# Kernel tuning notes

Measured on AMD Instinct MI355X. Metric: run time of the kernel, lower is better.

The kernel has to match this reference:

```python
import jax, jax.numpy as jnp
import numpy as np

B, S, H = 2, 1024, 64
DN, DR, DV = 128, 64, 128   # qk_nope, qk_rope, v head dims
QR, KR = 1536, 512          # q_lora_rank, kv_lora_rank
SCALE = 1.0 / float(np.sqrt(DN + DR))
NEG = jnp.float32(-1e30)


def _rope_tables(n, d):
    # matches gen_rope: theta over d/2 freqs, outer with positions, repeat(1,1,2) -> NeoX layout
    theta = 1.0 / (10000.0 ** (np.arange(0, d, 2, dtype=np.float32) / d))
    ang = np.arange(n, dtype=np.float32)[:, None] * theta[None, :]
    ang = np.tile(ang, (1, 2))  # [n, d]
    return jnp.asarray(np.cos(ang), jnp.float32), jnp.asarray(np.sin(ang), jnp.float32)


def setup_inputs() -> dict:
    key = jax.random.key(0)
    k0, k1, k2, k3, k4 = jax.random.split(key, 5)
    Q = jax.random.normal(k0, (B, S, QR), jnp.float32)
    KV = jax.random.normal(k1, (B, S, KR), jnp.float32)
    PE = jax.random.normal(k2, (B, S, DR), jnp.float32)
    WUQ = jax.random.normal(k3, (H * (DN + DR), QR), jnp.float32) / np.sqrt(QR)
    WUKV = jax.random.normal(k4, (H * (DN + DV), KR), jnp.float32) / np.sqrt(KR)
    cos, sin = _rope_tables(B * S, DR)  # [B*S, DR]
    return {"Q": Q, "KV": KV, "PE": PE, "WUQ": WUQ, "WUKV": WUKV, "cos": cos, "sin": sin}


def _rotate_half(x):
    h = x.shape[-1] // 2
    return jnp.concatenate([-x[..., h:], x[..., :h]], axis=-1)


def _apply_rope(x, cos, sin):
    return x * cos + _rotate_half(x) * sin


def reference(Q, KV, PE, WUQ, WUKV, cos, sin):
    cos = cos.reshape(B, S, DR)
    sin = sin.reshape(B, S, DR)
    # Q up-projection from latent: [B,S,QR] -> [B,S,H,DN+DR]
    q = jnp.einsum('bsr,dr->bsd', Q, WUQ).reshape(B, S, H, DN + DR)
    q_nope, q_pe = q[..., :DN], q[..., DN:]
    q_pe = _apply_rope(q_pe, cos[:, :, None, :], sin[:, :, None, :])
    # KV up-projection from latent: [B,S,KR] -> [B,S,H,DN+DV]
    kv = jnp.einsum('bsr,dr->bsd', KV, WUKV).reshape(B, S, H, DN + DV)
    k_nope, v = kv[..., :DN], kv[..., DN:]
    # decoupled rope key, shared across heads: [B,S,DR]
    k_pe = _apply_rope(PE, cos, sin)
    scores = (jnp.einsum('bqhd,bkhd->bhqk', q_nope, k_nope)
              + jnp.einsum('bqhd,bkd->bhqk', q_pe, k_pe)) * SCALE
    causal = jnp.tril(jnp.ones((S, S), dtype=bool))  # [S,S]
    scores = jnp.where(causal[None, None], scores, NEG)
    attn = jax.nn.softmax(scores, axis=-1)
    out = jnp.einsum('bhqk,bkhd->bqhd', attn, v)  # [B,S,H,DV]
    return out
```

## Files before the change

kernel.cpp:

```cpp
#include <hip/hip_runtime.h>
#include <math.h>

#define Bdim 2
#define Sdim 1024
#define Hdim 64
#define DN 128
#define DRr 64
#define DV 128
#define QRk 1536
#define KRk 512
#define Tn (Bdim*Sdim)
#define NQ (Hdim*(DN+DRr))
#define NKV (Hdim*(DN+DV))
#define SCALE 0.07216878364870323f

#define QB 128
#define KBLK 32
#define NTILE (Sdim/QB)
#define KSTR 200
#define VSTR 40
#define PSTR 40

typedef __bf16 bf16_t;
typedef bf16_t bf16x8 __attribute__((ext_vector_type(8)));
typedef float f32x4 __attribute__((ext_vector_type(4)));
typedef const __attribute__((address_space(1))) unsigned int* gas_ptr;
typedef __attribute__((address_space(3))) unsigned int* las_ptr;

__device__ __forceinline__ unsigned short f2bf(float f) {
  unsigned u = __builtin_bit_cast(unsigned, f);
  u += 0x7fffu + ((u >> 16) & 1u);
  return (unsigned short)(u >> 16);
}
__device__ __forceinline__ float bf2f(unsigned short h) {
  return __builtin_bit_cast(float, (unsigned)h << 16);
}

__global__ void cvt_f32_bf16(const float* __restrict__ in,
                             unsigned short* __restrict__ out, int n4) {
  int i = blockIdx.x * blockDim.x + threadIdx.x;
  int stride = gridDim.x * blockDim.x;
  for (int idx = i; idx < n4; idx += stride) {
    float4 v = reinterpret_cast<const float4*>(in)[idx];
    ushort4 o;
    o.x = f2bf(v.x); o.y = f2bf(v.y); o.z = f2bf(v.z); o.w = f2bf(v.w);
    reinterpret_cast<ushort4*>(out)[idx] = o;
  }
}

template<int EPI>
__global__ __launch_bounds__(256) void gemm_bt(
    const unsigned short* __restrict__ A, const unsigned short* __restrict__ B,
    unsigned short* __restrict__ C0, unsigned short* __restrict__ C1,
    int M, int N, int K)
{
  __shared__ __align__(16) unsigned short lds_a[128*32];
  __shared__ __align__(16) unsigned short lds_b[128*32];
  const int t  = threadIdx.x;
  const int l  = t & 63;
  const int w  = t >> 6;
  const int wr = (w >> 1) * 64;
  const int wc = (w & 1) * 64;
  const int by = blockIdx.y * 128;
  const int bx = blockIdx.x * 128;

  f32x4 acc[4][4];
#pragma unroll
  for (int m = 0; m < 4; ++m)
#pragma unroll
    for (int n = 0; n < 4; ++n) acc[m][n] = (f32x4){0.f,0.f,0.f,0.f};

  const int lr = t >> 2;
  const int lc = (t & 3) * 8;
  const unsigned short* Abase = A + (size_t)by * K + lc;
  const unsigned short* Bbase = B + (size_t)bx * K + lc;
  const int rl = l & 15;
  const int kl = (l >> 4) * 8;

  for (int k0 = 0; k0 < K; k0 += 32) {
#pragma unroll
    for (int i = 0; i < 2; ++i) {
      const unsigned short* ga = Abase + (size_t)(i*64 + lr) * K + k0;
      const unsigned short* gb = Bbase + (size_t)(i*64 + lr) * K + k0;
      __builtin_amdgcn_global_load_lds((gas_ptr)ga, (las_ptr)&lds_a[i*2048 + w*512], 16, 0, 0);
      __builtin_amdgcn_global_load_lds((gas_ptr)gb, (las_ptr)&lds_b[i*2048 + w*512], 16, 0, 0);
    }
    __syncthreads();
    bf16x8 af[4], bfv[4];
#pragma unroll
    for (int m = 0; m < 4; ++m)
      af[m] = *reinterpret_cast<const bf16x8*>(&lds_a[(wr + m*16 + rl)*32 + kl]);
#pragma unroll
    for (int n = 0; n < 4; ++n)
      bfv[n] = *reinterpret_cast<const bf16x8*>(&lds_b[(wc + n*16 + rl)*32 + kl]);
#pragma unroll
    for (int m = 0; m < 4; ++m)
#pragma unroll
      for (int n = 0; n < 4; ++n)
        acc[m][n] = __builtin_amdgcn_mfma_f32_16x16x32_bf16(af[m], bfv[n], acc[m][n], 0, 0, 0);
    __syncthreads();
  }

  const int rg = (l >> 4) * 4;
#pragma unroll
  for (int m = 0; m < 4; ++m)
#pragma unroll
    for (int n = 0; n < 4; ++n)
#pragma unroll
      for (int j = 0; j < 4; ++j) {
        int row = by + wr + m*16 + rg + j;
        int col = bx + wc + n*16 + rl;
        float v = acc[m][n][j];
        if constexpr (EPI == 0) {
          C0[(size_t)row * N + col] = f2bf(v);
        } else {
          int h = col >> 8;
          int d = col & 255;
          if (d < 128) {
            C0[(size_t)row * (Hdim*DN) + h*DN + d] = f2bf(v);
          } else {
            int bb = row >> 10;
            int tt = row & 1023;
            C1[(((size_t)(bb*Hdim + h) * DV + (d - 128)) << 10) + tt] = f2bf(v);
          }
        }
      }
}

__global__ void rope_q(unsigned short* __restrict__ q,
                       const float* __restrict__ cosb, const float* __restrict__ sinb) {
  int gid = blockIdx.x * blockDim.x + threadIdx.x;
  int wid = gid >> 6;
  int l = gid & 63;
  if (wid >= Tn * Hdim) return;
  int tt = wid >> 6;
  int h = wid & 63;
  unsigned short* row = q + (size_t)tt * NQ + h * (DN + DRr) + DN;
  float x = bf2f(row[l]);
  float other = __shfl_xor(x, 32, 64);
  float rot = (l < 32) ? -other : other;
  row[l] = f2bf(x * cosb[tt*64 + l] + rot * sinb[tt*64 + l]);
}

__global__ void rope_pe(const float* __restrict__ PE,
                        const float* __restrict__ cosb, const float* __restrict__ sinb,
                        unsigned short* __restrict__ kpe) {
  int gid = blockIdx.x * blockDim.x + threadIdx.x;
  int tt = gid >> 6;
  int l = gid & 63;
  if (tt >= Tn) return;
  float x = PE[tt*64 + l];
  float other = __shfl_xor(x, 32, 64);
  float rot = (l < 32) ? -other : other;
  kpe[tt*64 + l] = f2bf(x * cosb[tt*64 + l] + rot * sinb[tt*64 + l]);
}

__global__ __launch_bounds__(256, 2) void mla_attn(
    const unsigned short* __restrict__ qb,
    const unsigned short* __restrict__ kb,
    const unsigned short* __restrict__ pb,
    const unsigned short* __restrict__ vtb,
    float* __restrict__ out)
{
  const int bid = blockIdx.x;
  const int p  = bid & 3;
  const int h  = (bid >> 2) & 63;
  const int b  = bid >> 8;
  const int t  = threadIdx.x;
  const int w  = t >> 6;
  const int l  = t & 63;
  const int rl = l & 15;
  const int kl = (l >> 4) << 3;
  const int rg = (l >> 4) << 2;

  __shared__ __align__(16) unsigned short lds_k[KBLK*KSTR];
  __shared__ __align__(16) unsigned short lds_v[DV*VSTR];
  __shared__ __align__(16) unsigned short lds_p[4][2][16*PSTR];

  const int krow = t >> 3;
  const int kc8  = (t & 7) << 3;
  const int vrow = t >> 1;
  const int vc   = (t & 1) << 4;

  const unsigned short* kp = kb + (size_t)(b*Sdim)*(Hdim*DN) + h*DN;
  const unsigned short* pp = pb + (size_t)(b*Sdim)*DRr;
  const unsigned short* vp = vtb + (size_t)(b*Hdim + h)*DV*Sdim;

  for (int half = 0; half < 2; ++half) {
    const int tt = half ? (NTILE - 1 - p) : p;
    const int tb = tt * QB;
    const int nkt = (tb + QB) / KBLK;
    const int qw = tb + w*32;

    bf16x8 aq[2][6];
    const unsigned short* qp = qb + (size_t)(b*Sdim + qw) * NQ + h*(DN+DRr);
#pragma unroll
    for (int mb = 0; mb < 2; ++mb)
#pragma unroll
      for (int s = 0; s < 6; ++s)
        aq[mb][s] = *reinterpret_cast<const bf16x8*>(qp + (size_t)(mb*16 + rl)*NQ + s*32 + kl);

    f32x4 acc[2][8];
    f32x4 mrun[2], drun[2];
#pragma unroll
    for (int mb = 0; mb < 2; ++mb) {
#pragma unroll
      for (int v = 0; v < 8; ++v) acc[mb][v] = (f32x4){0.f,0.f,0.f,0.f};
#pragma unroll
      for (int j = 0; j < 4; ++j) { mrun[mb][j] = -INFINITY; drun[mb][j] = 0.f; }
    }

    for (int kt = 0; kt < nkt; ++kt) {
      const int kbase = kt * KBLK;
      {
        const unsigned short* krg = kp + (size_t)(kbase + krow)*(Hdim*DN);
        *reinterpret_cast<bf16x8*>(&lds_k[krow*KSTR + kc8]) =
            *reinterpret_cast<const bf16x8*>(krg + kc8);
        *reinterpret_cast<bf16x8*>(&lds_k[krow*KSTR + 64 + kc8]) =
            *reinterpret_cast<const bf16x8*>(krg + 64 + kc8);
        const unsigned short* prg = pp + (size_t)(kbase + krow)*DRr;
        *reinterpret_cast<bf16x8*>(&lds_k[krow*KSTR + 128 + kc8]) =
            *reinterpret_cast<const bf16x8*>(prg + kc8);
        const unsigned short* vrg = vp + (size_t)vrow*Sdim + kbase;
        *reinterpret_cast<bf16x8*>(&lds_v[vrow*VSTR + vc]) =
            *reinterpret_cast<const bf16x8*>(vrg + vc);
        *reinterpret_cast<bf16x8*>(&lds_v[vrow*VSTR + vc + 8]) =
            *reinterpret_cast<const bf16x8*>(vrg + vc + 8);
      }
      __syncthreads();

      f32x4 sc[2][2];
#pragma unroll
      for (int mb = 0; mb < 2; ++mb)
#pragma unroll
        for (int kh = 0; kh < 2; ++kh) sc[mb][kh] = (f32x4){0.f,0.f,0.f,0.f};
#pragma unroll
      for (int kh = 0; kh < 2; ++kh) {
        bf16x8 bk[6];
#pragma unroll
        for (int s = 0; s < 6; ++s)
          bk[s] = *reinterpret_cast<const bf16x8*>(&lds_k[(kh*16 + rl)*KSTR + s*32 + kl]);
#pragma unroll
        for (int mb = 0; mb < 2; ++mb)
#pragma unroll
          for (int s = 0; s < 6; ++s)
            sc[mb][kh] = __builtin_amdgcn_mfma_f32_16x16x32_bf16(aq[mb][s], bk[s], sc[mb][kh], 0, 0, 0);
      }

#pragma unroll
      for (int mb = 0; mb < 2; ++mb) {
#pragma unroll
        for (int kh = 0; kh < 2; ++kh) {
          const int key = kbase + kh*16 + rl;
#pragma unroll
          for (int j = 0; j < 4; ++j) {
            const int qrow = qw + mb*16 + rg + j;
            float sv = sc[mb][kh][j] * SCALE;
            sc[mb][kh][j] = (key <= qrow) ? sv : -INFINITY;
          }
        }
        f32x4 tm;
#pragma unroll
        for (int j = 0; j < 4; ++j) tm[j] = fmaxf(sc[mb][0][j], sc[mb][1][j]);
#pragma unroll
        for (int off = 1; off < 16; off <<= 1)
#pragma unroll
          for (int j = 0; j < 4; ++j) tm[j] = fmaxf(tm[j], __shfl_xor(tm[j], off, 64));
        f32x4 corr, ps;
#pragma unroll
        for (int j = 0; j < 4; ++j) {
          float mn = fmaxf(mrun[mb][j], tm[j]);
          corr[j] = __expf(mrun[mb][j] - mn);
          mrun[mb][j] = mn;
#pragma unroll
          for (int kh = 0; kh < 2; ++kh)
            sc[mb][kh][j] = __expf(sc[mb][kh][j] - mn);
          ps[j] = sc[mb][0][j] + sc[mb][1][j];
        }
#pragma unroll
        for (int off = 1; off < 16; off <<= 1)
#pragma unroll
          for (int j = 0; j < 4; ++j) ps[j] += __shfl_xor(ps[j], off, 64);
#pragma unroll
        for (int j = 0; j < 4; ++j) drun[mb][j] = drun[mb][j]*corr[j] + ps[j];
#pragma unroll
        for (int v = 0; v < 8; ++v)
#pragma unroll
          for (int j = 0; j < 4; ++j) acc[mb][v][j] *= corr[j];
#pragma unroll
        for (int kh = 0; kh < 2; ++kh)
#pragma unroll
          for (int j = 0; j < 4; ++j)
            lds_p[w][mb][(rg + j)*PSTR + kh*16 + rl] = f2bf(sc[mb][kh][j]);
      }

      bf16x8 ap[2];
#pragma unroll
      for (int mb = 0; mb < 2; ++mb)
        ap[mb] = *reinterpret_cast<const bf16x8*>(&lds_p[w][mb][rl*PSTR + kl]);
#pragma unroll
      for (int v = 0; v < 8; ++v) {
        bf16x8 bv = *reinterpret_cast<const bf16x8*>(&lds_v[(v*16 + rl)*VSTR + kl]);
#pragma unroll
        for (int mb = 0; mb < 2; ++mb)
          acc[mb][v] = __builtin_amdgcn_mfma_f32_16x16x32_bf16(ap[mb], bv, acc[mb][v], 0, 0, 0);
      }
      __syncthreads();
    }

#pragma unroll
    for (int mb = 0; mb < 2; ++mb) {
      f32x4 inv;
#pragma unroll
      for (int j = 0; j < 4; ++j) inv[j] = 1.f / drun[mb][j];
#pragma unroll
      for (int v = 0; v < 8; ++v)
#pragma unroll
        for (int j = 0; j < 4; ++j) {
          const int qrow = qw + mb*16 + rg + j;
          out[(((size_t)(b*Sdim + qrow))*Hdim + h)*DV + v*16 + rl] = acc[mb][v][j] * inv[j];
        }
    }
  }
}

extern "C" void kernel_launch(void* const* d_in, const int* in_sizes, int n_in,
                              void* d_out, int out_size, void* d_ws, size_t ws_size,
                              hipStream_t stream) {
  const float* Q    = (const float*)d_in[0];
  const float* KV   = (const float*)d_in[1];
  const float* PE   = (const float*)d_in[2];
  const float* WUQ  = (const float*)d_in[3];
  const float* WUKV = (const float*)d_in[4];
  const float* COS  = (const float*)d_in[5];
  const float* SIN  = (const float*)d_in[6];
  float* out = (float*)d_out;

  char* ws = (char*)d_ws;
  unsigned short* qbb   = (unsigned short*)(ws);
  unsigned short* wuqb  = (unsigned short*)(ws +   6291456);
  unsigned short* kvb   = (unsigned short*)(ws +  44040192);
  unsigned short* wukvb = (unsigned short*)(ws +  46137344);
  unsigned short* qbuf  = (unsigned short*)(ws +  62914560);
  unsigned short* kbuf  = (unsigned short*)(ws + 113246208);
  unsigned short* vtb   = (unsigned short*)(ws + 146800640);
  unsigned short* kpeb  = (unsigned short*)(ws + 180355072);

  cvt_f32_bf16<<<1024, 256, 0, stream>>>(Q,    qbb,   (Tn*QRk)/4);
  cvt_f32_bf16<<<2048, 256, 0, stream>>>(WUQ,  wuqb,  (NQ*QRk)/4);
  cvt_f32_bf16<<<512,  256, 0, stream>>>(KV,   kvb,   (Tn*KRk)/4);
  cvt_f32_bf16<<<1024, 256, 0, stream>>>(WUKV, wukvb, (NKV*KRk)/4);

  gemm_bt<0><<<dim3(NQ/128,  Tn/128), 256, 0, stream>>>(qbb, wuqb,  qbuf, (unsigned short*)nullptr, Tn, NQ,  QRk);
  gemm_bt<1><<<dim3(NKV/128, Tn/128), 256, 0, stream>>>(kvb, wukvb, kbuf, vtb,                      Tn, NKV, KRk);

  rope_q <<<(Tn*Hdim*64)/256, 256, 0, stream>>>(qbuf, COS, SIN);
  rope_pe<<<(Tn*64)/256,      256, 0, stream>>>(PE, COS, SIN, kpeb);

  mla_attn<<<Bdim*Hdim*4, 256, 0, stream>>>(qbuf, kbuf, kpeb, vtb, out);
}
```

Before: 516.5 us.

## Split attention into one block per query tile, heaviest first, with exp2 softmax

The attention kernel now launches one block per (query tile, batch, head) instead of pairing a light and a heavy causal tile inside each block. Blocks are ordered so the longest tiles start first, and launch bounds are raised to allow more resident blocks. The softmax moves to base 2 with the scale folded into one constant. It also skips the accumulator rescale when no row maximum grew across the wavefront. Raising the occupancy target may force register spilling, since each wave holds 32 accumulator vectors plus the Q fragments.

```diff
diff --git a/kernel.cpp b/kernel.cpp
--- a/kernel.cpp
+++ b/kernel.cpp
@@ -13,6 +13,7 @@
 #define NQ (Hdim*(DN+DRr))
 #define NKV (Hdim*(DN+DV))
 #define SCALE 0.07216878364870323f
+#define SC2 (SCALE * 1.4426950408889634f)
 
 #define QB 128
 #define KBLK 32
@@ -155,7 +156,7 @@
   kpe[tt*64 + l] = f2bf(x * cosb[tt*64 + l] + rot * sinb[tt*64 + l]);
 }
 
-__global__ __launch_bounds__(256, 2) void mla_attn(
+__global__ __launch_bounds__(256, 4) void mla_attn(
     const unsigned short* __restrict__ qb,
     const unsigned short* __restrict__ kb,
     const unsigned short* __restrict__ pb,
@@ -163,9 +164,10 @@
     float* __restrict__ out)
 {
   const int bid = blockIdx.x;
-  const int p  = bid & 3;
-  const int h  = (bid >> 2) & 63;
-  const int b  = bid >> 8;
+  const int bh  = bid & 127;
+  const int tile = (NTILE - 1) - (bid >> 7);
+  const int h  = bh & 63;
+  const int b  = bh >> 6;
   const int t  = threadIdx.x;
   const int w  = t >> 6;
   const int l  = t & 63;
@@ -186,95 +188,99 @@
   const unsigned short* pp = pb + (size_t)(b*Sdim)*DRr;
   const unsigned short* vp = vtb + (size_t)(b*Hdim + h)*DV*Sdim;
 
-  for (int half = 0; half < 2; ++half) {
-    const int tt = half ? (NTILE - 1 - p) : p;
-    const int tb = tt * QB;
-    const int nkt = (tb + QB) / KBLK;
-    const int qw = tb + w*32;
-
-    bf16x8 aq[2][6];
-    const unsigned short* qp = qb + (size_t)(b*Sdim + qw) * NQ + h*(DN+DRr);
+  const int tb = tile * QB;
+  const int nkt = (tb + QB) / KBLK;
+  const int qw = tb + w*32;
+
+  bf16x8 aq[2][6];
+  const unsigned short* qp = qb + (size_t)(b*Sdim + qw) * NQ + h*(DN+DRr);
+#pragma unroll
+  for (int mb = 0; mb < 2; ++mb)
+#pragma unroll
+    for (int s = 0; s < 6; ++s)
+      aq[mb][s] = *reinterpret_cast<const bf16x8*>(qp + (size_t)(mb*16 + rl)*NQ + s*32 + kl);
+
+  f32x4 acc[2][8];
+  f32x4 mrun[2], drun[2];
+#pragma unroll
+  for (int mb = 0; mb < 2; ++mb) {
+#pragma unroll
+    for (int v = 0; v < 8; ++v) acc[mb][v] = (f32x4){0.f,0.f,0.f,0.f};
+#pragma unroll
+    for (int j = 0; j < 4; ++j) { mrun[mb][j] = -INFINITY; drun[mb][j] = 0.f; }
+  }
+
+  for (int kt = 0; kt < nkt; ++kt) {
+    const int kbase = kt * KBLK;
+    {
+      const unsigned short* krg = kp + (size_t)(kbase + krow)*(Hdim*DN);
+      *reinterpret_cast<bf16x8*>(&lds_k[krow*KSTR + kc8]) =
+          *reinterpret_cast<const bf16x8*>(krg + kc8);
+      *reinterpret_cast<bf16x8*>(&lds_k[krow*KSTR + 64 + kc8]) =
+          *reinterpret_cast<const bf16x8*>(krg + 64 + kc8);
+      const unsigned short* prg = pp + (size_t)(kbase + krow)*DRr;
+      *reinterpret_cast<bf16x8*>(&lds_k[krow*KSTR + 128 + kc8]) =
+          *reinterpret_cast<const bf16x8*>(prg + kc8);
+      const unsigned short* vrg = vp + (size_t)vrow*Sdim + kbase;
+      *reinterpret_cast<bf16x8*>(&lds_v[vrow*VSTR + vc]) =
+          *reinterpret_cast<const bf16x8*>(vrg + vc);
+      *reinterpret_cast<bf16x8*>(&lds_v[vrow*VSTR + vc + 8]) =
+          *reinterpret_cast<const bf16x8*>(vrg + vc + 8);
+    }
+    __syncthreads();
+
+    f32x4 sc[2][2];
 #pragma unroll
     for (int mb = 0; mb < 2; ++mb)
 #pragma unroll
+      for (int kh = 0; kh < 2; ++kh) sc[mb][kh] = (f32x4){0.f,0.f,0.f,0.f};
+#pragma unroll
+    for (int kh = 0; kh < 2; ++kh) {
+      bf16x8 bk[6];
+#pragma unroll
       for (int s = 0; s < 6; ++s)
-        aq[mb][s] = *reinterpret_cast<const bf16x8*>(qp + (size_t)(mb*16 + rl)*NQ + s*32 + kl);
-
-    f32x4 acc[2][8];
-    f32x4 mrun[2], drun[2];
+        bk[s] = *reinterpret_cast<const bf16x8*>(&lds_k[(kh*16 + rl)*KSTR + s*32 + kl]);
+#pragma unroll
+      for (int mb = 0; mb < 2; ++mb)
+#pragma unroll
+        for (int s = 0; s < 6; ++s)
+          sc[mb][kh] = __builtin_amdgcn_mfma_f32_16x16x32_bf16(aq[mb][s], bk[s], sc[mb][kh], 0, 0, 0);
+    }
+
 #pragma unroll
     for (int mb = 0; mb < 2; ++mb) {
 #pragma unroll
-      for (int v = 0; v < 8; ++v) acc[mb][v] = (f32x4){0.f,0.f,0.f,0.f};
-#pragma unroll
-      for (int j = 0; j < 4; ++j) { mrun[mb][j] = -INFINITY; drun[mb][j] = 0.f; }
-    }
-
-    for (int kt = 0; kt < nkt; ++kt) {
-      const int kbase = kt * KBLK;
-      {
-        const unsigned short* krg = kp + (size_t)(kbase + krow)*(Hdim*DN);
-        *reinterpret_cast<bf16x8*>(&lds_k[krow*KSTR + kc8]) =
-            *reinterpret_cast<const bf16x8*>(krg + kc8);
-        *reinterpret_cast<bf16x8*>(&lds_k[krow*KSTR + 64 + kc8]) =
-            *reinterpret_cast<const bf16x8*>(krg + 64 + kc8);
-        const unsigned short* prg = pp + (size_t)(kbase + krow)*DRr;
-        *reinterpret_cast<bf16x8*>(&lds_k[krow*KSTR + 128 + kc8]) =
-            *reinterpret_cast<const bf16x8*>(prg + kc8);
-        const unsigned short* vrg = vp + (size_t)vrow*Sdim + kbase;
-        *reinterpret_cast<bf16x8*>(&lds_v[vrow*VSTR + vc]) =
-            *reinterpret_cast<const bf16x8*>(vrg + vc);
-        *reinterpret_cast<bf16x8*>(&lds_v[vrow*VSTR + vc + 8]) =
-            *reinterpret_cast<const bf16x8*>(vrg + vc + 8);
+      for (int kh = 0; kh < 2; ++kh) {
+        const int key = kbase + kh*16 + rl;
+#pragma unroll
+        for (int j = 0; j < 4; ++j) {
+          const int qrow = qw + mb*16 + rg + j;
+          float sv = sc[mb][kh][j] * SC2;
+          sc[mb][kh][j] = (key <= qrow) ? sv : -INFINITY;
+        }
       }
-      __syncthreads();
-
-      f32x4 sc[2][2];
-#pragma unroll
-      for (int mb = 0; mb < 2; ++mb)
-#pragma unroll
-        for (int kh = 0; kh < 2; ++kh) sc[mb][kh] = (f32x4){0.f,0.f,0.f,0.f};
-#pragma unroll
-      for (int kh = 0; kh < 2; ++kh) {
-        bf16x8 bk[6];
-#pragma unroll
-        for (int s = 0; s < 6; ++s)
-          bk[s] = *reinterpret_cast<const bf16x8*>(&lds_k[(kh*16 + rl)*KSTR + s*32 + kl]);
-#pragma unroll
-        for (int mb = 0; mb < 2; ++mb)
-#pragma unroll
-          for (int s = 0; s < 6; ++s)
-            sc[mb][kh] = __builtin_amdgcn_mfma_f32_16x16x32_bf16(aq[mb][s], bk[s], sc[mb][kh], 0, 0, 0);
-      }
-
-#pragma unroll
-      for (int mb = 0; mb < 2; ++mb) {
-#pragma unroll
-        for (int kh = 0; kh < 2; ++kh) {
-          const int key = kbase + kh*16 + rl;
-#pragma unroll
-          for (int j = 0; j < 4; ++j) {
-            const int qrow = qw + mb*16 + rg + j;
-            float sv = sc[mb][kh][j] * SCALE;
-            sc[mb][kh][j] = (key <= qrow) ? sv : -INFINITY;
-          }
-        }
-        f32x4 tm;
-#pragma unroll
-        for (int j = 0; j < 4; ++j) tm[j] = fmaxf(sc[mb][0][j], sc[mb][1][j]);
-#pragma unroll
-        for (int off = 1; off < 16; off <<= 1)
-#pragma unroll
-          for (int j = 0; j < 4; ++j) tm[j] = fmaxf(tm[j], __shfl_xor(tm[j], off, 64));
+      f32x4 tm;
+#pragma unroll
+      for (int j = 0; j < 4; ++j) tm[j] = fmaxf(sc[mb][0][j], sc[mb][1][j]);
+#pragma unroll
+      for (int off = 1; off < 16; off <<= 1)
+#pragma unroll
+        for (int j = 0; j < 4; ++j) tm[j] = fmaxf(tm[j], __shfl_xor(tm[j], off, 64));
+
+      int grow = 0;
+#pragma unroll
+      for (int j = 0; j < 4; ++j) grow |= (tm[j] > mrun[mb][j]) ? 1 : 0;
+
+      if (__any(grow)) {
         f32x4 corr, ps;
 #pragma unroll
         for (int j = 0; j < 4; ++j) {
           float mn = fmaxf(mrun[mb][j], tm[j]);
-          corr[j] = __expf(mrun[mb][j] - mn);
+          corr[j] = exp2f(mrun[mb][j] - mn);
           mrun[mb][j] = mn;
 #pragma unroll
           for (int kh = 0; kh < 2; ++kh)
-            sc[mb][kh][j] = __expf(sc[mb][kh][j] - mn);
+            sc[mb][kh][j] = exp2f(sc[mb][kh][j] - mn);
           ps[j] = sc[mb][0][j] + sc[mb][1][j];
         }
 #pragma unroll
@@ -287,40 +293,55 @@
         for (int v = 0; v < 8; ++v)
 #pragma unroll
           for (int j = 0; j < 4; ++j) acc[mb][v][j] *= corr[j];
-#pragma unroll
-        for (int kh = 0; kh < 2; ++kh)
-#pragma unroll
-          for (int j = 0; j < 4; ++j)
-            lds_p[w][mb][(rg + j)*PSTR + kh*16 + rl] = f2bf(sc[mb][kh][j]);
+      } else {
+        f32x4 ps;
+#pragma unroll
+        for (int j = 0; j < 4; ++j) {
+#pragma unroll
+          for (int kh = 0; kh < 2; ++kh)
+            sc[mb][kh][j] = exp2f(sc[mb][kh][j] - mrun[mb][j]);
+          ps[j] = sc[mb][0][j] + sc[mb][1][j];
+        }
+#pragma unroll
+        for (int off = 1; off < 16; off <<= 1)
+#pragma unroll
+          for (int j = 0; j < 4; ++j) ps[j] += __shfl_xor(ps[j], off, 64);
+#pragma unroll
+        for (int j = 0; j < 4; ++j) drun[mb][j] += ps[j];
       }
-
-      bf16x8 ap[2];
+#pragma unroll
+      for (int kh = 0; kh < 2; ++kh)
+#pragma unroll
+        for (int j = 0; j < 4; ++j)
+          lds_p[w][mb][(rg + j)*PSTR + kh*16 + rl] = f2bf(sc[mb][kh][j]);
+    }
+
+    bf16x8 ap[2];
+#pragma unroll
+    for (int mb = 0; mb < 2; ++mb)
+      ap[mb] = *reinterpret_cast<const bf16x8*>(&lds_p[w][mb][rl*PSTR + kl]);
+#pragma unroll
+    for (int v = 0; v < 8; ++v) {
+      bf16x8 bv = *reinterpret_cast<const bf16x8*>(&lds_v[(v*16 + rl)*VSTR + kl]);
 #pragma unroll
       for (int mb = 0; mb < 2; ++mb)
-        ap[mb] = *reinterpret_cast<const bf16x8*>(&lds_p[w][mb][rl*PSTR + kl]);
-#pragma unroll
-      for (int v = 0; v < 8; ++v) {
-        bf16x8 bv = *reinterpret_cast<const bf16x8*>(&lds_v[(v*16 + rl)*VSTR + kl]);
-#pragma unroll
-        for (int mb = 0; mb < 2; ++mb)
-          acc[mb][v] = __builtin_amdgcn_mfma_f32_16x16x32_bf16(ap[mb], bv, acc[mb][v], 0, 0, 0);
+        acc[mb][v] = __builtin_amdgcn_mfma_f32_16x16x32_bf16(ap[mb], bv, acc[mb][v], 0, 0, 0);
+    }
+    __syncthreads();
+  }
+
+#pragma unroll
+  for (int mb = 0; mb < 2; ++mb) {
+    f32x4 inv;
+#pragma unroll
+    for (int j = 0; j < 4; ++j) inv[j] = 1.f / drun[mb][j];
+#pragma unroll
+    for (int v = 0; v < 8; ++v)
+#pragma unroll
+      for (int j = 0; j < 4; ++j) {
+        const int qrow = qw + mb*16 + rg + j;
+        out[(((size_t)(b*Sdim + qrow))*Hdim + h)*DV + v*16 + rl] = acc[mb][v][j] * inv[j];
       }
-      __syncthreads();
-    }
-
-#pragma unroll
-    for (int mb = 0; mb < 2; ++mb) {
-      f32x4 inv;
-#pragma unroll
-      for (int j = 0; j < 4; ++j) inv[j] = 1.f / drun[mb][j];
-#pragma unroll
-      for (int v = 0; v < 8; ++v)
-#pragma unroll
-        for (int j = 0; j < 4; ++j) {
-          const int qrow = qw + mb*16 + rg + j;
-          out[(((size_t)(b*Sdim + qrow))*Hdim + h)*DV + v*16 + rl] = acc[mb][v][j] * inv[j];
-        }
-    }
   }
 }
 
@@ -357,5 +378,5 @@
   rope_q <<<(Tn*Hdim*64)/256, 256, 0, stream>>>(qbuf, COS, SIN);
   rope_pe<<<(Tn*64)/256,      256, 0, stream>>>(PE, COS, SIN, kpeb);
 
-  mla_attn<<<Bdim*Hdim*4, 256, 0, stream>>>(qbuf, kbuf, kpeb, vtb, out);
-}
+  mla_attn<<<NTILE*Bdim*Hdim, 256, 0, stream>>>(qbuf, kbuf, kpeb, vtb, out);
+}
```

Measured after the change: 877.0 us. 1.7x slower.
